# Kernel optimization log

Measured on AMD Instinct MI355X. Metric: run time of the kernel, lower is better.

Reference implementation:

```python
import jax, jax.numpy as jnp
import numpy as np

# Static config derived from img size 144 (min spatial dim > 128 branch):
SCALES = [9, 18, 36]            # kernel sizes (cubic)
WEIGHTS = [0.1, 0.3, 0.6]       # kernel weight ratios
DILATIONS = [2, 2, 2]
STRIDES = [max((k + 1) // 4, 1) for k in SCALES]  # [2, 4, 9]
EPS = 1e-5


def _box_sum(x, k, stride, dil):
    # Local sum over a dilated k^3 window, valid padding (matches F.conv3d
    # with an all-ones [1,1,k,k,k] kernel).
    kern = jnp.ones((1, 1, k, k, k), dtype=x.dtype)
    return jax.lax.conv_general_dilated(
        x, kern,
        window_strides=(stride,) * 3,
        padding='VALID',
        rhs_dilation=(dil,) * 3,
        dimension_numbers=('NCDHW', 'OIDHW', 'NCDHW'))


def setup_inputs() -> dict:
    key = jax.random.key(0)
    k1, k2 = jax.random.split(key)
    shape = (4, 1, 144, 144, 144)
    return {
        'input': jax.random.normal(k1, shape, dtype=jnp.float32),
        'target': jax.random.normal(k2, shape, dtype=jnp.float32),
    }


def reference(input, target):
    B = input.shape[0]
    input_2 = input * input
    target_2 = target * target
    input_target = input * target
    lncc_total = jnp.float32(0.0)
    for k, w, dil, st in zip(SCALES, WEIGHTS, DILATIONS, STRIDES):
        i_sum = _box_sum(input, k, st, dil).reshape(B, -1)
        t_sum = _box_sum(target, k, st, dil).reshape(B, -1)
        i2_sum = _box_sum(input_2, k, st, dil).reshape(B, -1)
        t2_sum = _box_sum(target_2, k, st, dil).reshape(B, -1)
        it_sum = _box_sum(input_target, k, st, dil).reshape(B, -1)
        numel = float(k ** 3)
        i_mean = i_sum / numel
        t_mean = t_sum / numel
        cross = it_sum - t_mean * i_sum - i_mean * t_sum + t_mean * i_mean * numel
        i_var = i2_sum - 2.0 * i_mean * i_sum + i_mean * i_mean * numel
        t_var = t2_sum - 2.0 * t_mean * t_sum + t_mean * t_mean * numel
        lncc = (cross * cross) / (i_var * t_var + EPS)
        lncc_total = lncc_total + w * (1.0 - lncc.mean())
    return lncc_total * B
```

## Files before the change

### kernel.cpp

```cpp
#include <hip/hip_runtime.h>


constexpr int BATCH = 4;
constexpr int DIM   = 144;
constexpr int NROWS = BATCH * DIM * DIM;
constexpr float EPS = 1e-5f;

constexpr int N1C  = NROWS * 9;
constexpr int N2Ae = BATCH * 72 * 64 * 64;
constexpr int N2Be = BATCH * 72 * 28 * 28;
constexpr int N2C  = BATCH * DIM * 9 * 9;


__device__ __forceinline__ float lncc_val(const float s[5], float inv_numel) {
    float cross = s[4] - s[0] * s[1] * inv_numel;
    float ivar  = s[2] - s[0] * s[0] * inv_numel;
    float tvar  = s[3] - s[1] * s[1] * inv_numel;
    return (cross * cross) / (ivar * tvar + EPS);
}

__device__ __forceinline__ void block_reduce_store(float acc, float* slot) {
    #pragma unroll
    for (int off = 32; off > 0; off >>= 1) acc += __shfl_down(acc, off, 64);
    __shared__ float sm[4];
    int lane = threadIdx.x & 63, wid = threadIdx.x >> 6;
    if (lane == 0) sm[wid] = acc;
    __syncthreads();
    if (threadIdx.x == 0) *slot = sm[0] + sm[1] + sm[2] + sm[3];
}


__device__ void aXY_body(int blk, const float* __restrict__ in,
                         const float* __restrict__ tg,
                         float* __restrict__ b2a, float* xs)
{
    const int p  = blk >> 2;
    const int c  = blk & 3;
    const int b  = p / 72;
    const int ez = p % 72;
    const int xo0 = c * 16;
    const size_t gpl = (size_t)(b * DIM + 2 * ez) * (DIM * DIM);
    const int t = threadIdx.x;

    for (int i = t; i < 576; i += 256) {
        int yp = i >> 3, dp = i & 7;
        int dx0 = dp * 2;
        int e0  = xo0 + dx0;
        const float* rowa = in + gpl + (size_t)(2 * yp) * DIM;
        const float* rowb = tg + gpl + (size_t)(2 * yp) * DIM;
        const float4* ga = (const float4*)rowa + (e0 >> 1);
        const float4* gb = (const float4*)rowb + (e0 >> 1);
        float ea[10], eb[10];
        #pragma unroll
        for (int k = 0; k < 5; ++k) {
            float4 A = ga[k]; ea[2 * k] = A.x; ea[2 * k + 1] = A.z;
            float4 B = gb[k]; eb[2 * k] = B.x; eb[2 * k + 1] = B.z;
        }
        float* xr = &xs[yp * 82 + dx0];
        #pragma unroll
        for (int q = 0; q < 5; ++q) {
            float2 sq; sq.x = 0.f; sq.y = 0.f;
            #pragma unroll
            for (int j = 0; j < 9; ++j) {
                float a0 = ea[j],     b0 = eb[j];
                float a1 = ea[j + 1], b1 = eb[j + 1];
                float v0, v1;
                if (q == 0)      { v0 = a0;      v1 = a1; }
                else if (q == 1) { v0 = b0;      v1 = b1; }
                else if (q == 2) { v0 = a0 * a0; v1 = a1 * a1; }
                else if (q == 3) { v0 = b0 * b0; v1 = b1 * b1; }
                else             { v0 = a0 * b0; v1 = a1 * b1; }
                sq.x += v0; sq.y += v1;
            }
            *(float2*)&xr[q * 16] = sq;
        }
    }
    __syncthreads();

    if (t < 160) {
        int dp = t & 7;
        int q  = (t >> 3) % 5;
        int ch = t / 40;
        int dx0 = 2 * dp, yo0 = ch * 16;
        const float2* xp2 = (const float2*)xs + ((q * 16 + dx0) >> 1);
        float2 s; s.x = 0.f; s.y = 0.f;
        #pragma unroll
        for (int j = 0; j < 9; ++j) {
            float2 v = xp2[(yo0 + j) * 41];
            s.x += v.x; s.y += v.y;
        }
        float2* ob = (float2*)(b2a + (size_t)q * N2Ae
                               + ((size_t)p * 64 + yo0) * 64 + xo0 + dx0);
        ob[0] = s;
        #pragma unroll
        for (int i2 = 1; i2 < 16; ++i2) {
            float2 vn = xp2[(yo0 + i2 + 8) * 41];
            float2 vo = xp2[(yo0 + i2 - 1) * 41];
            s.x += vn.x - vo.x; s.y += vn.y - vo.y;
            ob[(size_t)i2 * 32] = s;
        }
    }
}

constexpr int CXROWS   = 24;
constexpr int CXSTRIDE = 292;

__device__ void cX_body(int blk, const float* __restrict__ in,
                        const float* __restrict__ tg,
                        float* __restrict__ b1c, float* lv)
{
    const int t = threadIdx.x;
    const int row0 = blk * CXROWS;
    const float4* gin = (const float4*)(in + (size_t)row0 * DIM);
    const float4* gtg = (const float4*)(tg + (size_t)row0 * DIM);
    for (int i4 = t; i4 < CXROWS * 36; i4 += 256) {
        int rr = i4 / 36, k = i4 % 36;
        float4 A = gin[i4], B = gtg[i4];
        float4* d = (float4*)&lv[rr * CXSTRIDE + k * 8];
        float4 w0; w0.x = A.x; w0.y = B.x; w0.z = A.y; w0.w = B.y;
        float4 w1; w1.x = A.z; w1.y = B.z; w1.z = A.w; w1.w = B.w;
        d[0] = w0; d[1] = w1;
    }
    __syncthreads();
    if (t < CXROWS * 9) {
        int rr = t / 9, xo = t % 9;
        const float2* pp = (const float2*)&lv[rr * CXSTRIDE] + xo * 9;
        float s0 = 0.f, s1 = 0.f, s2 = 0.f, s3 = 0.f, s4 = 0.f;
        #pragma unroll
        for (int j = 0; j < 36; ++j) {
            float2 ab = pp[2 * j];
            float a = ab.x, bb = ab.y;
            s0 += a; s1 += bb; s2 += a * a; s3 += bb * bb; s4 += a * bb;
        }
        int o = (row0 + rr) * 9 + xo;
        b1c[o] = s0; b1c[N1C + o] = s1; b1c[2 * N1C + o] = s2;
        b1c[3 * N1C + o] = s3; b1c[4 * N1C + o] = s4;
    }
}

constexpr int B_AXY = BATCH * 72 * 4;
constexpr int B_CX  = NROWS / CXROWS;
constexpr int SM1   = CXROWS * CXSTRIDE;

__global__ __launch_bounds__(256) void k1(const float* __restrict__ in,
                                          const float* __restrict__ tg,
                                          float* __restrict__ b2a,
                                          float* __restrict__ b1c)
{
    __shared__ float smem[SM1];
    int blk = blockIdx.x;
    if (blk < B_AXY) aXY_body(blk, in, tg, b2a, smem);
    else             cX_body(blk - B_AXY, in, tg, b1c, smem);
}


__device__ __forceinline__ void aZ_body(int blk, const float* __restrict__ b2a,
                                        float* __restrict__ pA)
{
    int tid = blk * 256 + threadIdx.x;
    float acc = 0.f;
    {
        int xo = tid & 63;
        int yo = (tid >> 6) & 63;
        int ch = (tid >> 12) & 7;
        int b  = tid >> 15;
        const int zo0 = ch * 8;
        const int OO = 64 * 64;
        const float* base = b2a + (size_t)b * 72 * OO + yo * 64 + xo;

        float s[5] = {0.f, 0.f, 0.f, 0.f, 0.f};
        #pragma unroll
        for (int j = 0; j < 9; ++j) {
            #pragma unroll
            for (int q = 0; q < 5; ++q)
                s[q] += base[(size_t)q * N2Ae + (zo0 + j) * OO];
        }
        acc += lncc_val(s, 1.0f / 729.0f);
        #pragma unroll
        for (int i = 1; i < 8; ++i) {
            #pragma unroll
            for (int q = 0; q < 5; ++q)
                s[q] += base[(size_t)q * N2Ae + (zo0 + i + 8) * OO]
                      - base[(size_t)q * N2Ae + (zo0 + i - 1) * OO];
            acc += lncc_val(s, 1.0f / 729.0f);
        }
    }
    block_reduce_store(acc, pA + blk);
}

__device__ __forceinline__ void bXY_body(int tid, const float* __restrict__ b2a,
                                         float* __restrict__ b2b)
{
    const int total = BATCH * 72 * 28 * 28;
    if (tid >= total) return;
    int xo = tid % 28;
    int yo = (tid / 28) % 28;
    int p  = tid / 784;
    const float* ib = b2a + (size_t)p * 4096;
    float* ob = b2b + (size_t)p * 784 + yo * 28 + xo;
    int r0 = (2 * yo) * 64 + 2 * xo;
    #pragma unroll
    for (int q = 0; q < 5; ++q) {
        const float* pq = ib + (size_t)q * N2Ae;
        ob[(size_t)q * N2Be] =
            pq[r0] + pq[r0 + 9] + pq[r0 + 9 * 64] + pq[r0 + 9 * 64 + 9];
    }
}

__device__ __forceinline__ void cY_body(int tid, const float* __restrict__ b1c,
                                        float* __restrict__ b2c)
{
    const int total = BATCH * DIM * 9 * 9 * 8;
    if (tid >= total) return;
    int sp   = tid & 7;
    int rest = tid >> 3;
    int xo = rest % 9;
    int yo = (rest / 9) % 9;
    int bz = rest / 81;
    const float* base = b1c + (size_t)bz * DIM * 9 + xo;

    float s[5] = {0.f, 0.f, 0.f, 0.f, 0.f};
    #pragma unroll
    for (int j = 0; j < 36; ++j) {
        if ((j & 7) == sp) {
            int y = 9 * yo + 2 * j;
            #pragma unroll
            for (int q = 0; q < 5; ++q) s[q] += base[(size_t)q * N1C + y * 9];
        }
    }
    #pragma unroll
    for (int off = 1; off < 8; off <<= 1) {
        #pragma unroll
        for (int q = 0; q < 5; ++q) s[q] += __shfl_xor(s[q], off, 64);
    }
    if (sp == 0) {
        float* ob = b2c + (size_t)bz * 81 + yo * 9 + xo;
        #pragma unroll
        for (int q = 0; q < 5; ++q) ob[(size_t)q * N2C] = s[q];
    }
}

constexpr int B_AZ  = (BATCH * 8 * 64 * 64) / 256;
constexpr int B_BXY = (BATCH * 72 * 28 * 28) / 256;
constexpr int B_CY  = (BATCH * DIM * 9 * 9 * 8) / 256;

__global__ __launch_bounds__(256) void k2(const float* __restrict__ b2a,
                                          const float* __restrict__ b1c,
                                          float* __restrict__ b2b,
                                          float* __restrict__ b2c,
                                          float* __restrict__ pA)
{
    int blk = blockIdx.x;
    if (blk < B_AZ)              aZ_body(blk, b2a, pA);
    else if (blk < B_AZ + B_BXY) bXY_body((blk - B_AZ) * 256 + threadIdx.x, b2a, b2b);
    else                         cY_body((blk - B_AZ - B_BXY) * 256 + threadIdx.x, b1c, b2c);
}


__device__ __forceinline__ void bZ_body(int blk, const float* __restrict__ b2b,
                                        float* __restrict__ pB)
{
    int tid = blk * 256 + threadIdx.x;
    float acc = 0.f;
    {
        int sp   = tid & 7;
        int rest = tid >> 3;
        int xo = rest % 28;
        int yo = (rest / 28) % 28;
        int zo = (rest / 784) % 28;
        int b  = rest / 21952;
        const int OO = 784;
        const float* base = b2b + (size_t)b * 72 * OO + yo * 28 + xo;

        float s[5] = {0.f, 0.f, 0.f, 0.f, 0.f};
        #pragma unroll
        for (int j = 0; j < 18; ++j) {
            if ((j & 7) == sp) {
                #pragma unroll
                for (int q = 0; q < 5; ++q)
                    s[q] += base[(size_t)q * N2Be + (2 * zo + j) * OO];
            }
        }
        #pragma unroll
        for (int off = 1; off < 8; off <<= 1) {
            #pragma unroll
            for (int q = 0; q < 5; ++q) s[q] += __shfl_xor(s[q], off, 64);
        }
        if (sp == 0) acc = lncc_val(s, 1.0f / 5832.0f);
    }
    block_reduce_store(acc, pB + blk);
}

__device__ __forceinline__ void cZ_body(int blk, const float* __restrict__ b2c,
                                        float* __restrict__ pC)
{
    int tid = blk * 256 + threadIdx.x;
    const int total = BATCH * 9 * 9 * 9 * 16;
    float acc = 0.f;
    if (tid < total) {
        int sp   = tid & 15;
        int rest = tid >> 4;
        int xo = rest % 9;
        int yo = (rest / 9) % 9;
        int zo = (rest / 81) % 9;
        int b  = rest / 729;
        const int OO = 81;
        const float* base = b2c + (size_t)b * DIM * OO + yo * 9 + xo;

        float s[5] = {0.f, 0.f, 0.f, 0.f, 0.f};
        #pragma unroll
        for (int j = 0; j < 36; ++j) {
            if ((j & 15) == sp) {
                int z = 9 * zo + 2 * j;
                #pragma unroll
                for (int q = 0; q < 5; ++q) s[q] += base[(size_t)q * N2C + z * OO];
            }
        }
        #pragma unroll
        for (int off = 1; off < 16; off <<= 1) {
            #pragma unroll
            for (int q = 0; q < 5; ++q) s[q] += __shfl_xor(s[q], off, 64);
        }
        if (sp == 0) acc = lncc_val(s, 1.0f / 46656.0f);
    }
    block_reduce_store(acc, pC + blk);
}

constexpr int B_BZ = (BATCH * 28 * 28 * 28 * 8) / 256;
constexpr int B_CZ = (BATCH * 9 * 9 * 9 * 16 + 255) / 256;

__global__ __launch_bounds__(256) void k3(const float* __restrict__ b2b,
                                          const float* __restrict__ b2c,
                                          float* __restrict__ pB,
                                          float* __restrict__ pC)
{
    int blk = blockIdx.x;
    if (blk < B_BZ) bZ_body(blk, b2b, pB);
    else            cZ_body(blk - B_BZ, b2c, pC);
}


__global__ __launch_bounds__(256) void k4(const float* __restrict__ pA,
                                          const float* __restrict__ pB,
                                          const float* __restrict__ pC,
                                          float* __restrict__ out)
{
    const int t = threadIdx.x;
    float sA = 0.f, sB = 0.f, sC = 0.f;
    for (int i = t; i < B_AZ; i += 256) sA += pA[i];
    for (int i = t; i < B_BZ; i += 256) sB += pB[i];
    for (int i = t; i < B_CZ; i += 256) sC += pC[i];
    float s = (0.1f / 262144.0f) * sA + (0.3f / 21952.0f) * sB
            + (0.6f / 729.0f) * sC;
    #pragma unroll
    for (int off = 32; off > 0; off >>= 1) s += __shfl_down(s, off, 64);
    __shared__ float sm[4];
    int lane = t & 63, wid = t >> 6;
    if (lane == 0) sm[wid] = s;
    __syncthreads();
    if (t == 0) out[0] = 4.0f - (sm[0] + sm[1] + sm[2] + sm[3]);
}

extern "C" void kernel_launch(void* const* d_in, const int* in_sizes, int n_in,
                              void* d_out, int out_size, void* d_ws, size_t ws_size,
                              hipStream_t stream) {
    const float* input  = (const float*)d_in[0];
    const float* target = (const float*)d_in[1];
    float* out = (float*)d_out;

    float* b2a = (float*)d_ws;
    float* b1c = b2a + (size_t)5 * N2Ae;
    float* b2b = b1c + (size_t)5 * N1C;
    float* b2c = b2b + (size_t)5 * N2Be;
    float* pA  = b2c + (size_t)5 * N2C;
    float* pB  = pA + B_AZ;
    float* pC  = pB + B_BZ;

    k1<<<B_AXY + B_CX, 256, 0, stream>>>(input, target, b2a, b1c);
    k2<<<B_AZ + B_BXY + B_CY, 256, 0, stream>>>(b2a, b1c, b2b, b2c, pA);
    k3<<<B_BZ + B_CZ, 256, 0, stream>>>(b2b, b2c, pB, pC);
    k4<<<1, 256, 0, stream>>>(pA, pB, pC, out);
}
```

Baseline: 88.17 us.

## Rebalance kernel stages and vectorize B-scale XY and Z passes

Moves the scale-A Z reduction out of the second launch into the third, so the heavy A work runs alongside the B and C Z passes rather than alongside the lighter XY/Y passes. The B-scale XY pass now has each thread produce two adjacent outputs using float4 row loads, and the B-scale Z pass reads float2 pairs and evaluates two output columns per thread, halving its thread count. The shared-memory pass in k1 remaps its thread-to-(q, chunk) index to avoid modulo and division. This aims to balance work between launches and cut per-element load instructions, at the cost of more registers in the B Z pass.

Result: no change. 88.10 us (-0.1%).

```diff
diff --git a/kernel.cpp b/kernel.cpp
--- a/kernel.cpp
+++ b/kernel.cpp
@@ -79,8 +79,8 @@
 
     if (t < 160) {
         int dp = t & 7;
-        int q  = (t >> 3) % 5;
-        int ch = t / 40;
+        int ch = (t >> 3) & 3;
+        int q  = t >> 5;
         int dx0 = 2 * dp, yo0 = ch * 16;
         const float2* xp2 = (const float2*)xs + ((q * 16 + dx0) >> 1);
         float2 s; s.x = 0.f; s.y = 0.f;
@@ -154,6 +154,77 @@
 }
 
 
+__device__ __forceinline__ void bXY_body(int tid, const float* __restrict__ b2a,
+                                         float* __restrict__ b2b)
+{
+    const int total = BATCH * 72 * 28 * 14;
+    if (tid >= total) return;
+    int px = tid % 14;
+    int yo = (tid / 14) % 28;
+    int p  = tid / 392;
+    const float* ib = b2a + (size_t)p * 4096;
+    int r0 = 2 * yo * 64, r1 = r0 + 9 * 64;
+    #pragma unroll
+    for (int q = 0; q < 5; ++q) {
+        const float* pq = ib + (size_t)q * N2Ae;
+        const float4* row0 = (const float4*)(pq + r0);
+        const float4* row1 = (const float4*)(pq + r1);
+        float4 a0 = row0[px], b0 = row0[px + 2];
+        float4 a1 = row1[px], b1 = row1[px + 2];
+        float2 o;
+        o.x = a0.x + b0.y + a1.x + b1.y;
+        o.y = a0.z + b0.w + a1.z + b1.w;
+        *(float2*)(b2b + (size_t)q * N2Be + (size_t)p * 784 + yo * 28 + 2 * px) = o;
+    }
+}
+
+__device__ __forceinline__ void cY_body(int tid, const float* __restrict__ b1c,
+                                        float* __restrict__ b2c)
+{
+    const int total = BATCH * DIM * 9 * 9 * 8;
+    if (tid >= total) return;
+    int sp   = tid & 7;
+    int rest = tid >> 3;
+    int xo = rest % 9;
+    int yo = (rest / 9) % 9;
+    int bz = rest / 81;
+    const float* base = b1c + (size_t)bz * DIM * 9 + xo;
+
+    float s[5] = {0.f, 0.f, 0.f, 0.f, 0.f};
+    #pragma unroll
+    for (int j = 0; j < 36; ++j) {
+        if ((j & 7) == sp) {
+            int y = 9 * yo + 2 * j;
+            #pragma unroll
+            for (int q = 0; q < 5; ++q) s[q] += base[(size_t)q * N1C + y * 9];
+        }
+    }
+    #pragma unroll
+    for (int off = 1; off < 8; off <<= 1) {
+        #pragma unroll
+        for (int q = 0; q < 5; ++q) s[q] += __shfl_xor(s[q], off, 64);
+    }
+    if (sp == 0) {
+        float* ob = b2c + (size_t)bz * 81 + yo * 9 + xo;
+        #pragma unroll
+        for (int q = 0; q < 5; ++q) ob[(size_t)q * N2C] = s[q];
+    }
+}
+
+constexpr int B_BXY = (BATCH * 72 * 28 * 14) / 256;
+constexpr int B_CY  = (BATCH * DIM * 9 * 9 * 8) / 256;
+
+__global__ __launch_bounds__(256) void k2a(const float* __restrict__ b2a,
+                                           const float* __restrict__ b1c,
+                                           float* __restrict__ b2b,
+                                           float* __restrict__ b2c)
+{
+    int blk = blockIdx.x;
+    if (blk < B_BXY) bXY_body(blk * 256 + threadIdx.x, b2a, b2b);
+    else             cY_body((blk - B_BXY) * 256 + threadIdx.x, b1c, b2c);
+}
+
+
 __device__ __forceinline__ void aZ_body(int blk, const float* __restrict__ b2a,
                                         float* __restrict__ pA)
 {
@@ -188,75 +259,6 @@
     block_reduce_store(acc, pA + blk);
 }
 
-__device__ __forceinline__ void bXY_body(int tid, const float* __restrict__ b2a,
-                                         float* __restrict__ b2b)
-{
-    const int total = BATCH * 72 * 28 * 28;
-    if (tid >= total) return;
-    int xo = tid % 28;
-    int yo = (tid / 28) % 28;
-    int p  = tid / 784;
-    const float* ib = b2a + (size_t)p * 4096;
-    float* ob = b2b + (size_t)p * 784 + yo * 28 + xo;
-    int r0 = (2 * yo) * 64 + 2 * xo;
-    #pragma unroll
-    for (int q = 0; q < 5; ++q) {
-        const float* pq = ib + (size_t)q * N2Ae;
-        ob[(size_t)q * N2Be] =
-            pq[r0] + pq[r0 + 9] + pq[r0 + 9 * 64] + pq[r0 + 9 * 64 + 9];
-    }
-}
-
-__device__ __forceinline__ void cY_body(int tid, const float* __restrict__ b1c,
-                                        float* __restrict__ b2c)
-{
-    const int total = BATCH * DIM * 9 * 9 * 8;
-    if (tid >= total) return;
-    int sp   = tid & 7;
-    int rest = tid >> 3;
-    int xo = rest % 9;
-    int yo = (rest / 9) % 9;
-    int bz = rest / 81;
-    const float* base = b1c + (size_t)bz * DIM * 9 + xo;
-
-    float s[5] = {0.f, 0.f, 0.f, 0.f, 0.f};
-    #pragma unroll
-    for (int j = 0; j < 36; ++j) {
-        if ((j & 7) == sp) {
-            int y = 9 * yo + 2 * j;
-            #pragma unroll
-            for (int q = 0; q < 5; ++q) s[q] += base[(size_t)q * N1C + y * 9];
-        }
-    }
-    #pragma unroll
-    for (int off = 1; off < 8; off <<= 1) {
-        #pragma unroll
-        for (int q = 0; q < 5; ++q) s[q] += __shfl_xor(s[q], off, 64);
-    }
-    if (sp == 0) {
-        float* ob = b2c + (size_t)bz * 81 + yo * 9 + xo;
-        #pragma unroll
-        for (int q = 0; q < 5; ++q) ob[(size_t)q * N2C] = s[q];
-    }
-}
-
-constexpr int B_AZ  = (BATCH * 8 * 64 * 64) / 256;
-constexpr int B_BXY = (BATCH * 72 * 28 * 28) / 256;
-constexpr int B_CY  = (BATCH * DIM * 9 * 9 * 8) / 256;
-
-__global__ __launch_bounds__(256) void k2(const float* __restrict__ b2a,
-                                          const float* __restrict__ b1c,
-                                          float* __restrict__ b2b,
-                                          float* __restrict__ b2c,
-                                          float* __restrict__ pA)
-{
-    int blk = blockIdx.x;
-    if (blk < B_AZ)              aZ_body(blk, b2a, pA);
-    else if (blk < B_AZ + B_BXY) bXY_body((blk - B_AZ) * 256 + threadIdx.x, b2a, b2b);
-    else                         cY_body((blk - B_AZ - B_BXY) * 256 + threadIdx.x, b1c, b2c);
-}
-
-
 __device__ __forceinline__ void bZ_body(int blk, const float* __restrict__ b2b,
                                         float* __restrict__ pB)
 {
@@ -265,28 +267,36 @@
     {
         int sp   = tid & 7;
         int rest = tid >> 3;
-        int xo = rest % 28;
-        int yo = (rest / 28) % 28;
-        int zo = (rest / 784) % 28;
-        int b  = rest / 21952;
+        int px = rest % 14;
+        int yo = (rest / 14) % 28;
+        int zo = (rest / 392) % 28;
+        int b  = rest / 10976;
         const int OO = 784;
-        const float* base = b2b + (size_t)b * 72 * OO + yo * 28 + xo;
-
-        float s[5] = {0.f, 0.f, 0.f, 0.f, 0.f};
+        const float* base = b2b + (size_t)b * 72 * OO + yo * 28 + 2 * px;
+
+        float sx[5] = {0.f, 0.f, 0.f, 0.f, 0.f};
+        float sy[5] = {0.f, 0.f, 0.f, 0.f, 0.f};
         #pragma unroll
         for (int j = 0; j < 18; ++j) {
             if ((j & 7) == sp) {
                 #pragma unroll
-                for (int q = 0; q < 5; ++q)
-                    s[q] += base[(size_t)q * N2Be + (2 * zo + j) * OO];
+                for (int q = 0; q < 5; ++q) {
+                    float2 v = *(const float2*)(base + (size_t)q * N2Be
+                                                + (2 * zo + j) * OO);
+                    sx[q] += v.x; sy[q] += v.y;
+                }
             }
         }
         #pragma unroll
         for (int off = 1; off < 8; off <<= 1) {
             #pragma unroll
-            for (int q = 0; q < 5; ++q) s[q] += __shfl_xor(s[q], off, 64);
-        }
-        if (sp == 0) acc = lncc_val(s, 1.0f / 5832.0f);
+            for (int q = 0; q < 5; ++q) {
+                sx[q] += __shfl_xor(sx[q], off, 64);
+                sy[q] += __shfl_xor(sy[q], off, 64);
+            }
+        }
+        if (sp == 0)
+            acc = lncc_val(sx, 1.0f / 5832.0f) + lncc_val(sy, 1.0f / 5832.0f);
     }
     block_reduce_store(acc, pB + blk);
 }
@@ -326,17 +336,21 @@
     block_reduce_store(acc, pC + blk);
 }
 
-constexpr int B_BZ = (BATCH * 28 * 28 * 28 * 8) / 256;
+constexpr int B_AZ = (BATCH * 8 * 64 * 64) / 256;
+constexpr int B_BZ = (BATCH * 28 * 28 * 14 * 8) / 256;
 constexpr int B_CZ = (BATCH * 9 * 9 * 9 * 16 + 255) / 256;
 
-__global__ __launch_bounds__(256) void k3(const float* __restrict__ b2b,
-                                          const float* __restrict__ b2c,
-                                          float* __restrict__ pB,
-                                          float* __restrict__ pC)
+__global__ __launch_bounds__(256) void k2b(const float* __restrict__ b2a,
+                                           const float* __restrict__ b2b,
+                                           const float* __restrict__ b2c,
+                                           float* __restrict__ pA,
+                                           float* __restrict__ pB,
+                                           float* __restrict__ pC)
 {
     int blk = blockIdx.x;
-    if (blk < B_BZ) bZ_body(blk, b2b, pB);
-    else            cZ_body(blk - B_BZ, b2c, pC);
+    if (blk < B_AZ)             aZ_body(blk, b2a, pA);
+    else if (blk < B_AZ + B_BZ) bZ_body(blk - B_AZ, b2b, pB);
+    else                        cZ_body(blk - B_AZ - B_BZ, b2c, pC);
 }
 
 
@@ -377,7 +391,7 @@
     float* pC  = pB + B_BZ;
 
     k1<<<B_AXY + B_CX, 256, 0, stream>>>(input, target, b2a, b1c);
-    k2<<<B_AZ + B_BXY + B_CY, 256, 0, stream>>>(b2a, b1c, b2b, b2c, pA);
-    k3<<<B_BZ + B_CZ, 256, 0, stream>>>(b2b, b2c, pB, pC);
+    k2a<<<B_BXY + B_CY, 256, 0, stream>>>(b2a, b1c, b2b, b2c);
+    k2b<<<B_AZ + B_BZ + B_CZ, 256, 0, stream>>>(b2a, b2b, b2c, pA, pB, pC);
     k4<<<1, 256, 0, stream>>>(pA, pB, pC, out);
 }
```

## Fuse scale-B and scale-C Y/Z reductions into one kernel, dropping intermediate buffers

Applied to the files above, without the earlier changes.

Removes the separate bXY/bZ and cY/cZ passes and their intermediate buffers. Scale-B now sums the 3D window straight from the b2a partials, and scale-C reduces a whole 36x36 y/z window per wavefront from b1c. This cuts one kernel launch and the b2b/b2c global write and read round trips. In exchange, more redundant global loads happen per output, with scattered access patterns. It also reorders the thread-to-(q,ch) mapping in the aXY stage.

Measured after the change: 132.3 us. 50.0% more time.

```diff
diff --git a/kernel.cpp b/kernel.cpp
--- a/kernel.cpp
+++ b/kernel.cpp
@@ -8,8 +8,6 @@
 
 constexpr int N1C  = NROWS * 9;
 constexpr int N2Ae = BATCH * 72 * 64 * 64;
-constexpr int N2Be = BATCH * 72 * 28 * 28;
-constexpr int N2C  = BATCH * DIM * 9 * 9;
 
 
 __device__ __forceinline__ float lncc_val(const float s[5], float inv_numel) {
@@ -79,8 +77,8 @@
 
     if (t < 160) {
         int dp = t & 7;
-        int q  = (t >> 3) % 5;
-        int ch = t / 40;
+        int ch = (t >> 3) & 3;
+        int q  = t >> 5;
         int dx0 = 2 * dp, yo0 = ch * 16;
         const float2* xp2 = (const float2*)xs + ((q * 16 + dx0) >> 1);
         float2 s; s.x = 0.f; s.y = 0.f;
@@ -154,193 +152,130 @@
 }
 
 
-__device__ __forceinline__ void aZ_body(int blk, const float* __restrict__ b2a,
-                                        float* __restrict__ pA)
-{
-    int tid = blk * 256 + threadIdx.x;
+__device__ __forceinline__ float bZdir_acc(int tid, const float* __restrict__ b2a)
+{
+    const int NG = BATCH * 28 * 28 * 4;
+    int gid  = tid >> 6;
+    int lane = tid & 63;
     float acc = 0.f;
-    {
-        int xo = tid & 63;
-        int yo = (tid >> 6) & 63;
-        int ch = (tid >> 12) & 7;
-        int b  = tid >> 15;
-        const int zo0 = ch * 8;
-        const int OO = 64 * 64;
-        const float* base = b2a + (size_t)b * 72 * OO + yo * 64 + xo;
-
+    if (gid < NG) {
+        int xh = gid & 3;
+        int r1 = gid >> 2;
+        int yo = r1 % 28;
+        int r2 = r1 / 28;
+        int zo = r2 % 28;
+        int b  = r2 / 28;
+        int sp = lane >> 3, xl = lane & 7;
+        int xo = xh * 8 + xl;
         float s[5] = {0.f, 0.f, 0.f, 0.f, 0.f};
-        #pragma unroll
-        for (int j = 0; j < 9; ++j) {
+        if (xo < 28) {
+            const float* base = b2a + (size_t)b * 72 * 4096 + (2 * yo) * 64 + 2 * xo;
+            const float* p0 = base + (size_t)(2 * zo + sp) * 4096;
+            const float* p1 = p0 + 8 * 4096;
             #pragma unroll
-            for (int q = 0; q < 5; ++q)
-                s[q] += base[(size_t)q * N2Ae + (zo0 + j) * OO];
-        }
+            for (int q = 0; q < 5; ++q) {
+                const float* a0 = p0 + (size_t)q * N2Ae;
+                const float* a1 = p1 + (size_t)q * N2Ae;
+                s[q] = a0[0] + a0[9] + a0[576] + a0[585]
+                     + a1[0] + a1[9] + a1[576] + a1[585];
+            }
+            if (sp < 2) {
+                const float* p2 = p1 + 8 * 4096;
+                #pragma unroll
+                for (int q = 0; q < 5; ++q) {
+                    const float* a2 = p2 + (size_t)q * N2Ae;
+                    s[q] += a2[0] + a2[9] + a2[576] + a2[585];
+                }
+            }
+        }
+        #pragma unroll
+        for (int off = 8; off < 64; off <<= 1) {
+            #pragma unroll
+            for (int q = 0; q < 5; ++q) s[q] += __shfl_xor(s[q], off, 64);
+        }
+        if (sp == 0 && xo < 28) acc = lncc_val(s, 1.0f / 5832.0f);
+    }
+    return acc;
+}
+
+__device__ __forceinline__ float aZ_acc(int tid, const float* __restrict__ b2a)
+{
+    int xo = tid & 63;
+    int yo = (tid >> 6) & 63;
+    int ch = (tid >> 12) & 7;
+    int b  = tid >> 15;
+    const int zo0 = ch * 8;
+    const int OO = 64 * 64;
+    const float* base = b2a + (size_t)b * 72 * OO + yo * 64 + xo;
+
+    float s[5] = {0.f, 0.f, 0.f, 0.f, 0.f};
+    #pragma unroll
+    for (int j = 0; j < 9; ++j) {
+        #pragma unroll
+        for (int q = 0; q < 5; ++q)
+            s[q] += base[(size_t)q * N2Ae + (zo0 + j) * OO];
+    }
+    float acc = lncc_val(s, 1.0f / 729.0f);
+    #pragma unroll
+    for (int i = 1; i < 8; ++i) {
+        #pragma unroll
+        for (int q = 0; q < 5; ++q)
+            s[q] += base[(size_t)q * N2Ae + (zo0 + i + 8) * OO]
+                  - base[(size_t)q * N2Ae + (zo0 + i - 1) * OO];
         acc += lncc_val(s, 1.0f / 729.0f);
-        #pragma unroll
-        for (int i = 1; i < 8; ++i) {
-            #pragma unroll
-            for (int q = 0; q < 5; ++q)
-                s[q] += base[(size_t)q * N2Ae + (zo0 + i + 8) * OO]
-                      - base[(size_t)q * N2Ae + (zo0 + i - 1) * OO];
-            acc += lncc_val(s, 1.0f / 729.0f);
-        }
-    }
-    block_reduce_store(acc, pA + blk);
-}
-
-__device__ __forceinline__ void bXY_body(int tid, const float* __restrict__ b2a,
-                                         float* __restrict__ b2b)
-{
-    const int total = BATCH * 72 * 28 * 28;
-    if (tid >= total) return;
-    int xo = tid % 28;
-    int yo = (tid / 28) % 28;
-    int p  = tid / 784;
-    const float* ib = b2a + (size_t)p * 4096;
-    float* ob = b2b + (size_t)p * 784 + yo * 28 + xo;
-    int r0 = (2 * yo) * 64 + 2 * xo;
-    #pragma unroll
-    for (int q = 0; q < 5; ++q) {
-        const float* pq = ib + (size_t)q * N2Ae;
-        ob[(size_t)q * N2Be] =
-            pq[r0] + pq[r0 + 9] + pq[r0 + 9 * 64] + pq[r0 + 9 * 64 + 9];
-    }
-}
-
-__device__ __forceinline__ void cY_body(int tid, const float* __restrict__ b1c,
-                                        float* __restrict__ b2c)
-{
-    const int total = BATCH * DIM * 9 * 9 * 8;
-    if (tid >= total) return;
-    int sp   = tid & 7;
-    int rest = tid >> 3;
-    int xo = rest % 9;
-    int yo = (rest / 9) % 9;
-    int bz = rest / 81;
-    const float* base = b1c + (size_t)bz * DIM * 9 + xo;
+    }
+    return acc;
+}
+
+__device__ __forceinline__ float cYZ_acc(int tid, const float* __restrict__ b1c)
+{
+    int gid  = tid >> 6;
+    int lane = tid & 63;
+    int xo = gid % 9;
+    int yo = (gid / 9) % 9;
+    int zo = (gid / 81) % 9;
+    int b  = gid / 729;
 
     float s[5] = {0.f, 0.f, 0.f, 0.f, 0.f};
-    #pragma unroll
-    for (int j = 0; j < 36; ++j) {
-        if ((j & 7) == sp) {
-            int y = 9 * yo + 2 * j;
-            #pragma unroll
-            for (int q = 0; q < 5; ++q) s[q] += base[(size_t)q * N1C + y * 9];
-        }
-    }
-    #pragma unroll
-    for (int off = 1; off < 8; off <<= 1) {
+    for (int j = lane; j < 1296; j += 64) {
+        int zj = j / 36;
+        int yj = j - zj * 36;
+        int idx = ((b * DIM + 9 * zo + 2 * zj) * DIM + 9 * yo + 2 * yj) * 9 + xo;
+        #pragma unroll
+        for (int q = 0; q < 5; ++q) s[q] += b1c[(size_t)q * N1C + idx];
+    }
+    #pragma unroll
+    for (int off = 1; off < 64; off <<= 1) {
         #pragma unroll
         for (int q = 0; q < 5; ++q) s[q] += __shfl_xor(s[q], off, 64);
     }
-    if (sp == 0) {
-        float* ob = b2c + (size_t)bz * 81 + yo * 9 + xo;
-        #pragma unroll
-        for (int q = 0; q < 5; ++q) ob[(size_t)q * N2C] = s[q];
-    }
-}
-
+    return (lane == 0) ? lncc_val(s, 1.0f / 46656.0f) : 0.f;
+}
+
+constexpr int B_BZD = (BATCH * 28 * 28 * 4 * 64) / 256;
 constexpr int B_AZ  = (BATCH * 8 * 64 * 64) / 256;
-constexpr int B_BXY = (BATCH * 72 * 28 * 28) / 256;
-constexpr int B_CY  = (BATCH * DIM * 9 * 9 * 8) / 256;
+constexpr int B_CYZ = (BATCH * 9 * 9 * 9 * 64) / 256;
 
 __global__ __launch_bounds__(256) void k2(const float* __restrict__ b2a,
                                           const float* __restrict__ b1c,
-                                          float* __restrict__ b2b,
-                                          float* __restrict__ b2c,
-                                          float* __restrict__ pA)
+                                          float* __restrict__ pB,
+                                          float* __restrict__ pA,
+                                          float* __restrict__ pC)
 {
     int blk = blockIdx.x;
-    if (blk < B_AZ)              aZ_body(blk, b2a, pA);
-    else if (blk < B_AZ + B_BXY) bXY_body((blk - B_AZ) * 256 + threadIdx.x, b2a, b2b);
-    else                         cY_body((blk - B_AZ - B_BXY) * 256 + threadIdx.x, b1c, b2c);
-}
-
-
-__device__ __forceinline__ void bZ_body(int blk, const float* __restrict__ b2b,
-                                        float* __restrict__ pB)
-{
-    int tid = blk * 256 + threadIdx.x;
-    float acc = 0.f;
-    {
-        int sp   = tid & 7;
-        int rest = tid >> 3;
-        int xo = rest % 28;
-        int yo = (rest / 28) % 28;
-        int zo = (rest / 784) % 28;
-        int b  = rest / 21952;
-        const int OO = 784;
-        const float* base = b2b + (size_t)b * 72 * OO + yo * 28 + xo;
-
-        float s[5] = {0.f, 0.f, 0.f, 0.f, 0.f};
-        #pragma unroll
-        for (int j = 0; j < 18; ++j) {
-            if ((j & 7) == sp) {
-                #pragma unroll
-                for (int q = 0; q < 5; ++q)
-                    s[q] += base[(size_t)q * N2Be + (2 * zo + j) * OO];
-            }
-        }
-        #pragma unroll
-        for (int off = 1; off < 8; off <<= 1) {
-            #pragma unroll
-            for (int q = 0; q < 5; ++q) s[q] += __shfl_xor(s[q], off, 64);
-        }
-        if (sp == 0) acc = lncc_val(s, 1.0f / 5832.0f);
-    }
-    block_reduce_store(acc, pB + blk);
-}
-
-__device__ __forceinline__ void cZ_body(int blk, const float* __restrict__ b2c,
-                                        float* __restrict__ pC)
-{
-    int tid = blk * 256 + threadIdx.x;
-    const int total = BATCH * 9 * 9 * 9 * 16;
-    float acc = 0.f;
-    if (tid < total) {
-        int sp   = tid & 15;
-        int rest = tid >> 4;
-        int xo = rest % 9;
-        int yo = (rest / 9) % 9;
-        int zo = (rest / 81) % 9;
-        int b  = rest / 729;
-        const int OO = 81;
-        const float* base = b2c + (size_t)b * DIM * OO + yo * 9 + xo;
-
-        float s[5] = {0.f, 0.f, 0.f, 0.f, 0.f};
-        #pragma unroll
-        for (int j = 0; j < 36; ++j) {
-            if ((j & 15) == sp) {
-                int z = 9 * zo + 2 * j;
-                #pragma unroll
-                for (int q = 0; q < 5; ++q) s[q] += base[(size_t)q * N2C + z * OO];
-            }
-        }
-        #pragma unroll
-        for (int off = 1; off < 16; off <<= 1) {
-            #pragma unroll
-            for (int q = 0; q < 5; ++q) s[q] += __shfl_xor(s[q], off, 64);
-        }
-        if (sp == 0) acc = lncc_val(s, 1.0f / 46656.0f);
-    }
-    block_reduce_store(acc, pC + blk);
-}
-
-constexpr int B_BZ = (BATCH * 28 * 28 * 28 * 8) / 256;
-constexpr int B_CZ = (BATCH * 9 * 9 * 9 * 16 + 255) / 256;
-
-__global__ __launch_bounds__(256) void k3(const float* __restrict__ b2b,
-                                          const float* __restrict__ b2c,
-                                          float* __restrict__ pB,
-                                          float* __restrict__ pC)
-{
-    int blk = blockIdx.x;
-    if (blk < B_BZ) bZ_body(blk, b2b, pB);
-    else            cZ_body(blk - B_BZ, b2c, pC);
-}
-
-
-__global__ __launch_bounds__(256) void k4(const float* __restrict__ pA,
+    if (blk < B_BZD) {
+        block_reduce_store(bZdir_acc(blk * 256 + threadIdx.x, b2a), pB + blk);
+    } else if (blk < B_BZD + B_AZ) {
+        int bb = blk - B_BZD;
+        block_reduce_store(aZ_acc(bb * 256 + threadIdx.x, b2a), pA + bb);
+    } else {
+        int cb = blk - B_BZD - B_AZ;
+        block_reduce_store(cYZ_acc(cb * 256 + threadIdx.x, b1c), pC + cb);
+    }
+}
+
+
+__global__ __launch_bounds__(256) void k3(const float* __restrict__ pA,
                                           const float* __restrict__ pB,
                                           const float* __restrict__ pC,
                                           float* __restrict__ out)
@@ -348,8 +283,8 @@
     const int t = threadIdx.x;
     float sA = 0.f, sB = 0.f, sC = 0.f;
     for (int i = t; i < B_AZ; i += 256) sA += pA[i];
-    for (int i = t; i < B_BZ; i += 256) sB += pB[i];
-    for (int i = t; i < B_CZ; i += 256) sC += pC[i];
+    for (int i = t; i < B_BZD; i += 256) sB += pB[i];
+    for (int i = t; i < B_CYZ; i += 256) sC += pC[i];
     float s = (0.1f / 262144.0f) * sA + (0.3f / 21952.0f) * sB
             + (0.6f / 729.0f) * sC;
     #pragma unroll
@@ -370,14 +305,11 @@
 
     float* b2a = (float*)d_ws;
     float* b1c = b2a + (size_t)5 * N2Ae;
-    float* b2b = b1c + (size_t)5 * N1C;
-    float* b2c = b2b + (size_t)5 * N2Be;
-    float* pA  = b2c + (size_t)5 * N2C;
-    float* pB  = pA + B_AZ;
-    float* pC  = pB + B_BZ;
+    float* pB  = b1c + (size_t)5 * N1C;
+    float* pA  = pB + B_BZD;
+    float* pC  = pA + B_AZ;
 
     k1<<<B_AXY + B_CX, 256, 0, stream>>>(input, target, b2a, b1c);
-    k2<<<B_AZ + B_BXY + B_CY, 256, 0, stream>>>(b2a, b1c, b2b, b2c, pA);
-    k3<<<B_BZ + B_CZ, 256, 0, stream>>>(b2b, b2c, pB, pC);
-    k4<<<1, 256, 0, stream>>>(pA, pB, pC, out);
-}
+    k2<<<B_BZD + B_AZ + B_CYZ, 256, 0, stream>>>(b2a, b1c, pB, pA, pC);
+    k3<<<1, 256, 0, stream>>>(pA, pB, pC, out);
+}
```
